# Optimization experiments

Hardware: AMD Instinct MI355X
Metric: run time of the kernel (lower is better)

Reference implementation:

```python
import jax, jax.numpy as jnp
import numpy as np

N_NODES = 50000
N_EDGES = 1600000
D_IN = 64
D_OUT = 64
N_REL = 6


def setup_inputs() -> dict:
    key = jax.random.key(0)
    k = jax.random.split(key, 6)
    x = jax.random.normal(k[0], (N_NODES, D_IN), dtype=jnp.float32)
    edge_index = jax.random.randint(k[1], (2, N_EDGES), 0, N_NODES, dtype=jnp.int32)
    edge_type = jax.random.randint(k[2], (N_EDGES,), 0, N_REL, dtype=jnp.int32)
    # RGCN parameters: per-relation weight, root (self-loop) weight, bias
    W = jax.random.normal(k[3], (N_REL, D_IN, D_OUT), dtype=jnp.float32) / np.float32(np.sqrt(D_IN))
    root = jax.random.normal(k[4], (D_IN, D_OUT), dtype=jnp.float32) / np.float32(np.sqrt(D_IN))
    bias = jnp.zeros((D_OUT,), dtype=jnp.float32)
    return {"x": x, "W": W, "root": root, "bias": bias,
            "edge_index": edge_index, "edge_type": edge_type}


def reference(x, W, root, bias, edge_index, edge_type):
    """RGCNConv forward (PyG semantics, default aggr='mean' per relation):
    out[i] = bias + x[i] @ root + sum_r mean_{j in N_r(i)} (x[j] @ W_r)
    """
    src, dst = edge_index[0], edge_index[1]
    # Transform all node features by all relation weights: [R, N, D_OUT]
    xr = jnp.einsum('nd,rdo->rno', x, W)
    # Per-edge message: relation-specific transformed source feature [E, D_OUT]
    m = xr[edge_type, src]
    # Mean normalization per (dst node, relation): 1 / #relation-r in-edges of dst
    seg = dst.astype(jnp.int32) * N_REL + edge_type.astype(jnp.int32)
    count = jax.ops.segment_sum(jnp.ones((m.shape[0],), x.dtype), seg,
                                num_segments=N_NODES * N_REL)
    norm = jnp.where(count > 0, 1.0 / jnp.maximum(count, 1.0), 0.0)
    m = m * norm[seg][:, None]
    # Scatter-add aggregation over destination nodes
    agg = jax.ops.segment_sum(m, dst, num_segments=N_NODES)
    return agg + x @ root + bias
```

## Files before the change

kernel.cpp:

```cpp
#include <hip/hip_runtime.h>

#define NN 50000
#define NE 1600000
#define D 64
#define NR 6
#define NSEG (NN * NR)
#define SB 512
#define BFRAG_N (4 * 14 * 64 * 8)
#define EPB 6400
#define NBLK1 (NE / EPB)
#define BUKSH 9
#define NBUK ((NSEG + 511) >> 9)
#define NG (NBUK * NBLK1)
#define SNB1 ((NG + SB - 1) / SB)
#define PREPB ((NN * D / 8 + 255) / 256)

typedef __attribute__((ext_vector_type(8))) short short8;
typedef __attribute__((ext_vector_type(4))) float f32x4;

__device__ __forceinline__ unsigned short f2bf(float f) {
    unsigned int u = __float_as_uint(f);
    unsigned int r = (u + 0x7FFF + ((u >> 16) & 1)) >> 16;
    return (unsigned short)r;
}

__global__ __launch_bounds__(256) void prep_hist_k(const float* __restrict__ x,
                                                   const float* __restrict__ W,
                                                   const float* __restrict__ root,
                                                   const int* __restrict__ dsts,
                                                   const int* __restrict__ et,
                                                   int* __restrict__ ghist,
                                                   unsigned short* __restrict__ xh,
                                                   unsigned short* __restrict__ Bfrag) {
    __shared__ int lh[NBUK];
    int tid = threadIdx.x;
    if (blockIdx.x < NBLK1) {
        int blk = blockIdx.x;
        for (int i = tid; i < NBUK; i += 256) lh[i] = 0;
        __syncthreads();
        int base = blk * EPB;
#pragma unroll 5
        for (int i = 0; i < EPB / 256; ++i) {
            int e = base + i * 256 + tid;
            int seg = dsts[e] * NR + et[e];
            atomicAdd(&lh[seg >> BUKSH], 1);
        }
        __syncthreads();
        for (int i = tid; i < NBUK; i += 256) ghist[i * NBLK1 + blk] = lh[i];
    } else {
        int t = (blockIdx.x - NBLK1) * 256 + tid;
        if (t < NN * D / 8) {
            const float4* xp = (const float4*)(x + (size_t)t * 8);
            float4 va = xp[0], vb = xp[1];
            uint4 o;
            o.x = (unsigned int)f2bf(va.x) | ((unsigned int)f2bf(va.y) << 16);
            o.y = (unsigned int)f2bf(va.z) | ((unsigned int)f2bf(va.w) << 16);
            o.z = (unsigned int)f2bf(vb.x) | ((unsigned int)f2bf(vb.y) << 16);
            o.w = (unsigned int)f2bf(vb.z) | ((unsigned int)f2bf(vb.w) << 16);
            *(uint4*)(xh + (size_t)t * 8) = o;
        }
        if (t < BFRAG_N) {
            int j = t & 7;
            int lane = (t >> 3) & 63;
            int rest = t >> 9;
            int ks = rest % 14;
            int nt = rest / 14;
            int k = ks * 32 + ((lane >> 4) * 8) + j;
            int n = nt * 16 + (lane & 15);
            float v = (k < 384) ? W[(size_t)k * 64 + n] : root[(size_t)(k - 384) * 64 + n];
            Bfrag[t] = f2bf(v);
        }
    }
}

__global__ void scanA_k(const int* __restrict__ v, int* __restrict__ incl,
                        int* __restrict__ blocksum, int n) {
    __shared__ int s[SB];
    int t = threadIdx.x, i = blockIdx.x * SB + t;
    s[t] = (i < n) ? v[i] : 0;
    __syncthreads();
    for (int off = 1; off < SB; off <<= 1) {
        int u = (t >= off) ? s[t - off] : 0;
        __syncthreads();
        s[t] += u;
        __syncthreads();
    }
    if (i < n) incl[i] = s[t];
    if (t == SB - 1) blocksum[blockIdx.x] = s[t];
}

__global__ void scanB_k(const int* __restrict__ blocksum, int* __restrict__ blockoff, int nb) {
    __shared__ int s[1024];
    int t = threadIdx.x;
    s[t] = (t < nb) ? blocksum[t] : 0;
    __syncthreads();
    for (int off = 1; off < 1024; off <<= 1) {
        int u = (t >= off) ? s[t - off] : 0;
        __syncthreads();
        s[t] += u;
        __syncthreads();
    }
    if (t < nb) blockoff[t] = s[t];
}

__global__ void scanC2_k(const int* __restrict__ incl, const int* __restrict__ blockoff,
                         const int* __restrict__ v, int* __restrict__ excl, int n) {
    int i = blockIdx.x * blockDim.x + threadIdx.x;
    if (i >= n) return;
    int b = i / SB;
    int Ri = incl[i] + (b > 0 ? blockoff[b - 1] : 0);
    excl[i] = Ri - v[i];
}

__global__ __launch_bounds__(256) void scatter1_k(const int* __restrict__ srcs,
                                                  const int* __restrict__ dsts,
                                                  const int* __restrict__ et,
                                                  const int* __restrict__ goff,
                                                  uint2* __restrict__ kv) {
    __shared__ int cur[NBUK];
    int tid = threadIdx.x, blk = blockIdx.x;
    for (int i = tid; i < NBUK; i += 256) cur[i] = goff[i * NBLK1 + blk];
    __syncthreads();
    int base = blk * EPB;
#pragma unroll 5
    for (int i = 0; i < EPB / 256; ++i) {
        int e = base + i * 256 + tid;
        int seg = dsts[e] * NR + et[e];
        int pos = atomicAdd(&cur[seg >> BUKSH], 1);
        kv[pos] = make_uint2((unsigned int)srcs[e] << 7, (unsigned int)seg);
    }
}

__global__ __launch_bounds__(256) void bucket2_k(const uint2* __restrict__ kv,
                                                 const int* __restrict__ goff,
                                                 int* __restrict__ rowstart,
                                                 int* __restrict__ pay) {
    __shared__ int h[512];
    __shared__ int part[256];
    int tid = threadIdx.x, b = blockIdx.x;
    int base = goff[b * NBLK1];
    int end  = (b + 1 < NBUK) ? goff[(b + 1) * NBLK1] : NE;
    for (int i = tid; i < 512; i += 256) h[i] = 0;
    __syncthreads();
    for (int k = base + tid; k < end; k += 256)
        atomicAdd(&h[kv[k].y & 511], 1);
    __syncthreads();
    int c0 = h[2 * tid], c1 = h[2 * tid + 1];
    part[tid] = c0 + c1;
    __syncthreads();
    for (int off = 1; off < 256; off <<= 1) {
        int u = (tid >= off) ? part[tid - off] : 0;
        __syncthreads();
        part[tid] += u;
        __syncthreads();
    }
    int pbase = (tid > 0) ? part[tid - 1] : 0;
    __syncthreads();
    int e0 = pbase, e1 = pbase + c0;
    h[2 * tid] = e0; h[2 * tid + 1] = e1;
    int segb = b << BUKSH;
    if (segb + 2 * tid     < NSEG) rowstart[segb + 2 * tid]     = base + e0;
    if (segb + 2 * tid + 1 < NSEG) rowstart[segb + 2 * tid + 1] = base + e1;
    if (b == 0 && tid == 0) rowstart[NSEG] = NE;
    __syncthreads();
    for (int k = base + tid; k < end; k += 256) {
        uint2 v = kv[k];
        int pos = base + atomicAdd(&h[v.y & 511], 1);
        pay[pos] = (int)v.x;
    }
}

__global__ __launch_bounds__(256) void agg13_k(const unsigned short* __restrict__ xh,
                                               const int* __restrict__ rowstart,
                                               const int* __restrict__ pay,
                                               unsigned short* __restrict__ Amain) {
    int wv = (blockIdx.x * blockDim.x + threadIdx.x) >> 6;
    int lane = threadIdx.x & 63;
    int g = lane >> 3;
    int q = lane & 7;
    int seg = 8 * wv + g;
    int k0 = rowstart[seg], k1 = rowstart[seg + 1];
    const char* xb = (const char*)xh;
    unsigned int qo = (unsigned int)q << 4;
    float a0 = 0.f, a1 = 0.f, a2 = 0.f, a3 = 0.f;
    float a4 = 0.f, a5 = 0.f, a6 = 0.f, a7 = 0.f;
    int len = k1 - k0;
    int k = k0;
    int k4 = k0 + (len & ~3);
    for (; k < k4; k += 4) {
        unsigned int pv[4];
#pragma unroll
        for (int j = 0; j < 4; ++j) pv[j] = (unsigned int)pay[k + j];
        uint4 uv[4];
#pragma unroll
        for (int j = 0; j < 4; ++j)
            uv[j] = *(const uint4*)(xb + pv[j] + qo);
#pragma unroll
        for (int j = 0; j < 4; ++j) {
            a0 += __uint_as_float(uv[j].x << 16);
            a1 += __uint_as_float(uv[j].x & 0xFFFF0000u);
            a2 += __uint_as_float(uv[j].y << 16);
            a3 += __uint_as_float(uv[j].y & 0xFFFF0000u);
            a4 += __uint_as_float(uv[j].z << 16);
            a5 += __uint_as_float(uv[j].z & 0xFFFF0000u);
            a6 += __uint_as_float(uv[j].w << 16);
            a7 += __uint_as_float(uv[j].w & 0xFFFF0000u);
        }
    }
    if (k < k1) {
        unsigned int pv[3];
        float mv[3];
#pragma unroll
        for (int j = 0; j < 3; ++j) {
            int kk = k + j;
            bool v = kk < k1;
            mv[j] = v ? 1.0f : 0.0f;
            pv[j] = (unsigned int)pay[v ? kk : k];
        }
#pragma unroll
        for (int j = 0; j < 3; ++j) {
            uint4 u = *(const uint4*)(xb + pv[j] + qo);
            a0 += __uint_as_float(u.x << 16) * mv[j];
            a1 += __uint_as_float(u.x & 0xFFFF0000u) * mv[j];
            a2 += __uint_as_float(u.y << 16) * mv[j];
            a3 += __uint_as_float(u.y & 0xFFFF0000u) * mv[j];
            a4 += __uint_as_float(u.z << 16) * mv[j];
            a5 += __uint_as_float(u.z & 0xFFFF0000u) * mv[j];
            a6 += __uint_as_float(u.w << 16) * mv[j];
            a7 += __uint_as_float(u.w & 0xFFFF0000u) * mv[j];
        }
    }
    float nrm = (len > 0) ? 1.0f / (float)len : 0.0f;
    uint4 o;
    o.x = (unsigned int)f2bf(a0 * nrm) | ((unsigned int)f2bf(a1 * nrm) << 16);
    o.y = (unsigned int)f2bf(a2 * nrm) | ((unsigned int)f2bf(a3 * nrm) << 16);
    o.z = (unsigned int)f2bf(a4 * nrm) | ((unsigned int)f2bf(a5 * nrm) << 16);
    o.w = (unsigned int)f2bf(a6 * nrm) | ((unsigned int)f2bf(a7 * nrm) << 16);
    *(uint4*)((char*)Amain + (size_t)seg * 128 + qo) = o;
}

__global__ __launch_bounds__(256) void mix4_k(const unsigned short* __restrict__ Amain,
                                              const unsigned short* __restrict__ xh,
                                              const unsigned short* __restrict__ Bfrag,
                                              const float* __restrict__ bias,
                                              float* __restrict__ out) {
    int t = threadIdx.x;
    int lane = t & 63;
    int w = t >> 6;
    int rowb = blockIdx.x * 64 + w * 16;
    int arow = rowb + (lane & 15);
    if (arow >= NN) arow = NN - 1;
    int ko = (lane >> 4) * 8;
    const unsigned short* ap = Amain + (size_t)arow * 384 + ko;
    const unsigned short* xp = xh + (size_t)arow * 64 + ko;
    const short8* bp = (const short8*)Bfrag + lane;
    f32x4 acc0 = {0.f, 0.f, 0.f, 0.f};
    f32x4 acc1 = acc0, acc2 = acc0, acc3 = acc0;
#pragma unroll
    for (int ks = 0; ks < 14; ++ks) {
        short8 a = (ks < 12) ? *(const short8*)(ap + ks * 32)
                             : *(const short8*)(xp + (ks - 12) * 32);
        short8 b0 = bp[(0 * 14 + ks) * 64];
        short8 b1 = bp[(1 * 14 + ks) * 64];
        short8 b2 = bp[(2 * 14 + ks) * 64];
        short8 b3 = bp[(3 * 14 + ks) * 64];
        acc0 = __builtin_amdgcn_mfma_f32_16x16x32_bf16(a, b0, acc0, 0, 0, 0);
        acc1 = __builtin_amdgcn_mfma_f32_16x16x32_bf16(a, b1, acc1, 0, 0, 0);
        acc2 = __builtin_amdgcn_mfma_f32_16x16x32_bf16(a, b2, acc2, 0, 0, 0);
        acc3 = __builtin_amdgcn_mfma_f32_16x16x32_bf16(a, b3, acc3, 0, 0, 0);
    }
    int col = lane & 15;
    int rout = rowb + (lane >> 4) * 4;
    float bv0 = bias[0 * 16 + col];
    float bv1 = bias[1 * 16 + col];
    float bv2 = bias[2 * 16 + col];
    float bv3 = bias[3 * 16 + col];
#pragma unroll
    for (int j = 0; j < 4; ++j) {
        int rr = rout + j;
        if (rr < NN) {
            float* op = out + (size_t)rr * 64;
            op[0 * 16 + col] = acc0[j] + bv0;
            op[1 * 16 + col] = acc1[j] + bv1;
            op[2 * 16 + col] = acc2[j] + bv2;
            op[3 * 16 + col] = acc3[j] + bv3;
        }
    }
}

__global__ void zero_i32_k(int* __restrict__ p, int n) {
    int i = blockIdx.x * blockDim.x + threadIdx.x;
    if (i < n) p[i] = 0;
}

__global__ void count_edges_k(const int* __restrict__ dst, const int* __restrict__ et,
                              int* __restrict__ cnt) {
    int e = blockIdx.x * blockDim.x + threadIdx.x;
    if (e < NE) atomicAdd(&cnt[dst[e] * NR + et[e]], 1);
}

__global__ void make_norm_k(const int* __restrict__ cnt, float* __restrict__ norm, int n) {
    int i = blockIdx.x * blockDim.x + threadIdx.x;
    if (i < n) {
        int c = cnt[i];
        norm[i] = (c > 0) ? 1.0f / (float)c : 0.0f;
    }
}

__global__ void init_out_k(const float* __restrict__ x, const float* __restrict__ root,
                           const float* __restrict__ bias, float* __restrict__ out) {
    int t = blockIdx.x * blockDim.x + threadIdx.x;
    int n = t >> 6;
    int o = t & 63;
    if (n >= NN) return;
    const float* xrow = x + n * D;
    float acc = bias[o];
#pragma unroll
    for (int d = 0; d < D; ++d) acc = fmaf(xrow[d], root[d * D + o], acc);
    out[t] = acc;
}

__global__ void scatter_mv_k(const int* __restrict__ srcs, const int* __restrict__ dsts,
                             const int* __restrict__ et, const float* __restrict__ x,
                             const float* __restrict__ W, const float* __restrict__ norm,
                             float* __restrict__ out) {
    int t = blockIdx.x * blockDim.x + threadIdx.x;
    int e = t >> 6;
    int o = t & 63;
    if (e >= NE) return;
    int s = srcs[e];
    int d2 = dsts[e];
    int r = et[e];
    float nrm = norm[d2 * NR + r];
    const float* xrow = x + s * D;
    const float* Wr = W + r * D * D + o;
    float acc = 0.0f;
#pragma unroll
    for (int d = 0; d < D; ++d) acc = fmaf(xrow[d], Wr[d * D], acc);
    atomicAdd(&out[d2 * D + o], acc * nrm);
}

extern "C" void kernel_launch(void* const* d_in, const int* in_sizes, int n_in,
                              void* d_out, int out_size, void* d_ws, size_t ws_size,
                              hipStream_t stream) {
    const float* x    = (const float*)d_in[0];
    const float* W    = (const float*)d_in[1];
    const float* root = (const float*)d_in[2];
    const float* bias = (const float*)d_in[3];
    const int*   ei   = (const int*)d_in[4];
    const int*   et   = (const int*)d_in[5];
    float* out = (float*)d_out;
    const int* srcs = ei;
    const int* dsts = ei + NE;

    char* ws = (char*)d_ws;
    size_t off = 0;
    int*   rowstart = (int*)(ws + off); off += (size_t)(NSEG + 1) * 4;
    int*   pay      = (int*)(ws + off); off += (size_t)NE * 4;
    off = (off + 255) & ~(size_t)255;
    uint2* kv       = (uint2*)(ws + off); off += (size_t)NE * 8;
    int*   ghist    = (int*)(ws + off); off += (size_t)NG * 4;
    int*   incl     = (int*)(ws + off); off += (size_t)NG * 4;
    int*   goff     = (int*)(ws + off); off += (size_t)NG * 4;
    int*   blocksum = (int*)(ws + off); off += (size_t)SNB1 * 4;
    int*   blockoff = (int*)(ws + off); off += (size_t)SNB1 * 4;
    off = (off + 255) & ~(size_t)255;
    unsigned short* Bfrag = (unsigned short*)(ws + off); off += (size_t)BFRAG_N * 2;
    off = (off + 255) & ~(size_t)255;
    unsigned short* xh = (unsigned short*)(ws + off); off += (size_t)NN * D * 2;
    off = (off + 255) & ~(size_t)255;
    unsigned short* Amain = (unsigned short*)(ws + off); off += (size_t)NN * 384 * 2;
    bool big = ws_size >= off;

    if (big) {
        prep_hist_k<<<NBLK1 + PREPB, 256, 0, stream>>>(x, W, root, dsts, et, ghist, xh, Bfrag);
        scanA_k<<<SNB1, SB, 0, stream>>>(ghist, incl, blocksum, NG);
        scanB_k<<<1, 1024, 0, stream>>>(blocksum, blockoff, SNB1);
        scanC2_k<<<(NG + 255) / 256, 256, 0, stream>>>(incl, blockoff, ghist, goff, NG);
        scatter1_k<<<NBLK1, 256, 0, stream>>>(srcs, dsts, et, goff, kv);
        bucket2_k<<<NBUK, 256, 0, stream>>>(kv, goff, rowstart, pay);
        int aggwaves = NSEG / 8;
        agg13_k<<<((size_t)aggwaves * 64 + 255) / 256, 256, 0, stream>>>(xh, rowstart, pay, Amain);
        mix4_k<<<(NN + 63) / 64, 256, 0, stream>>>(Amain, xh, Bfrag, bias, out);
    } else {
        int* cnt2  = (int*)(ws);
        float* norm = (float*)(ws + (size_t)NSEG * 4);
        zero_i32_k<<<(NSEG + 255) / 256, 256, 0, stream>>>(cnt2, NSEG);
        count_edges_k<<<(NE + 255) / 256, 256, 0, stream>>>(dsts, et, cnt2);
        make_norm_k<<<(NSEG + 255) / 256, 256, 0, stream>>>(cnt2, norm, NSEG);
        init_out_k<<<((size_t)NN * 64 + 255) / 256, 256, 0, stream>>>(x, root, bias, out);
        scatter_mv_k<<<((size_t)NE * 64 + 255) / 256, 256, 0, stream>>>(srcs, dsts, et, x, W, norm, out);
    }
}
```

Before: 96.75 us.

## Halve bucket width and process 16 segments per wave in aggregation

Bucket size for the two-level counting sort drops from 512 to 256 segments, which doubles the bucket count and makes each bucket2 block use one histogram slot per thread. The aggregation kernel now gives each segment to 4 lanes, each loading two 16-byte chunks, so one wave covers 16 segments instead of 8. This targets divergence from uneven segment lengths and raises memory-level parallelism per lane. In exchange it uses more registers per lane, doubles the number of global histogram groups to scan, and lengthens the scan path.

```diff
diff --git a/kernel.cpp b/kernel.cpp
--- a/kernel.cpp
+++ b/kernel.cpp
@@ -9,11 +9,12 @@
 #define BFRAG_N (4 * 14 * 64 * 8)
 #define EPB 6400
 #define NBLK1 (NE / EPB)
-#define BUKSH 9
-#define NBUK ((NSEG + 511) >> 9)
+#define BUKSH 8
+#define NBUK ((NSEG + 255) >> 8)
 #define NG (NBUK * NBLK1)
 #define SNB1 ((NG + SB - 1) / SB)
 #define PREPB ((NN * D / 8 + 255) / 256)
+#define AGGW (NSEG / 16)
 
 typedef __attribute__((ext_vector_type(8))) short short8;
 typedef __attribute__((ext_vector_type(4))) float f32x4;
@@ -23,6 +24,8 @@
     unsigned int r = (u + 0x7FFF + ((u >> 16) & 1)) >> 16;
     return (unsigned short)r;
 }
+__device__ __forceinline__ float bflo(unsigned int w) { return __uint_as_float(w << 16); }
+__device__ __forceinline__ float bfhi(unsigned int w) { return __uint_as_float(w & 0xFFFF0000u); }
 
 __global__ __launch_bounds__(256) void prep_hist_k(const float* __restrict__ x,
                                                    const float* __restrict__ W,
@@ -135,18 +138,18 @@
                                                  const int* __restrict__ goff,
                                                  int* __restrict__ rowstart,
                                                  int* __restrict__ pay) {
-    __shared__ int h[512];
+    __shared__ int h[256];
     __shared__ int part[256];
     int tid = threadIdx.x, b = blockIdx.x;
     int base = goff[b * NBLK1];
     int end  = (b + 1 < NBUK) ? goff[(b + 1) * NBLK1] : NE;
-    for (int i = tid; i < 512; i += 256) h[i] = 0;
+    h[tid] = 0;
     __syncthreads();
     for (int k = base + tid; k < end; k += 256)
-        atomicAdd(&h[kv[k].y & 511], 1);
-    __syncthreads();
-    int c0 = h[2 * tid], c1 = h[2 * tid + 1];
-    part[tid] = c0 + c1;
+        atomicAdd(&h[kv[k].y & 255], 1);
+    __syncthreads();
+    int c0 = h[tid];
+    part[tid] = c0;
     __syncthreads();
     for (int off = 1; off < 256; off <<= 1) {
         int u = (tid >= off) ? part[tid - off] : 0;
@@ -154,36 +157,36 @@
         part[tid] += u;
         __syncthreads();
     }
-    int pbase = (tid > 0) ? part[tid - 1] : 0;
-    __syncthreads();
-    int e0 = pbase, e1 = pbase + c0;
-    h[2 * tid] = e0; h[2 * tid + 1] = e1;
+    int e0 = part[tid] - c0;
+    __syncthreads();
+    h[tid] = e0;
     int segb = b << BUKSH;
-    if (segb + 2 * tid     < NSEG) rowstart[segb + 2 * tid]     = base + e0;
-    if (segb + 2 * tid + 1 < NSEG) rowstart[segb + 2 * tid + 1] = base + e1;
+    if (segb + tid < NSEG) rowstart[segb + tid] = base + e0;
     if (b == 0 && tid == 0) rowstart[NSEG] = NE;
     __syncthreads();
     for (int k = base + tid; k < end; k += 256) {
         uint2 v = kv[k];
-        int pos = base + atomicAdd(&h[v.y & 511], 1);
+        int pos = base + atomicAdd(&h[v.y & 255], 1);
         pay[pos] = (int)v.x;
     }
 }
 
-__global__ __launch_bounds__(256) void agg13_k(const unsigned short* __restrict__ xh,
+__global__ __launch_bounds__(256) void agg14_k(const unsigned short* __restrict__ xh,
                                                const int* __restrict__ rowstart,
                                                const int* __restrict__ pay,
                                                unsigned short* __restrict__ Amain) {
     int wv = (blockIdx.x * blockDim.x + threadIdx.x) >> 6;
+    if (wv >= AGGW) return;
     int lane = threadIdx.x & 63;
-    int g = lane >> 3;
-    int q = lane & 7;
-    int seg = 8 * wv + g;
+    int g = lane >> 2;
+    int q = lane & 3;
+    int seg = 16 * wv + g;
     int k0 = rowstart[seg], k1 = rowstart[seg + 1];
     const char* xb = (const char*)xh;
-    unsigned int qo = (unsigned int)q << 4;
-    float a0 = 0.f, a1 = 0.f, a2 = 0.f, a3 = 0.f;
-    float a4 = 0.f, a5 = 0.f, a6 = 0.f, a7 = 0.f;
+    unsigned int qo = (unsigned int)q << 5;
+    float acc[16];
+#pragma unroll
+    for (int c = 0; c < 16; ++c) acc[c] = 0.f;
     int len = k1 - k0;
     int k = k0;
     int k4 = k0 + (len & ~3);
@@ -191,20 +194,22 @@
         unsigned int pv[4];
 #pragma unroll
         for (int j = 0; j < 4; ++j) pv[j] = (unsigned int)pay[k + j];
-        uint4 uv[4];
-#pragma unroll
-        for (int j = 0; j < 4; ++j)
+        uint4 uv[4], vv[4];
+#pragma unroll
+        for (int j = 0; j < 4; ++j) {
             uv[j] = *(const uint4*)(xb + pv[j] + qo);
+            vv[j] = *(const uint4*)(xb + pv[j] + qo + 16);
+        }
 #pragma unroll
         for (int j = 0; j < 4; ++j) {
-            a0 += __uint_as_float(uv[j].x << 16);
-            a1 += __uint_as_float(uv[j].x & 0xFFFF0000u);
-            a2 += __uint_as_float(uv[j].y << 16);
-            a3 += __uint_as_float(uv[j].y & 0xFFFF0000u);
-            a4 += __uint_as_float(uv[j].z << 16);
-            a5 += __uint_as_float(uv[j].z & 0xFFFF0000u);
-            a6 += __uint_as_float(uv[j].w << 16);
-            a7 += __uint_as_float(uv[j].w & 0xFFFF0000u);
+            acc[0]  += bflo(uv[j].x); acc[1]  += bfhi(uv[j].x);
+            acc[2]  += bflo(uv[j].y); acc[3]  += bfhi(uv[j].y);
+            acc[4]  += bflo(uv[j].z); acc[5]  += bfhi(uv[j].z);
+            acc[6]  += bflo(uv[j].w); acc[7]  += bfhi(uv[j].w);
+            acc[8]  += bflo(vv[j].x); acc[9]  += bfhi(vv[j].x);
+            acc[10] += bflo(vv[j].y); acc[11] += bfhi(vv[j].y);
+            acc[12] += bflo(vv[j].z); acc[13] += bfhi(vv[j].z);
+            acc[14] += bflo(vv[j].w); acc[15] += bfhi(vv[j].w);
         }
     }
     if (k < k1) {
@@ -220,23 +225,30 @@
 #pragma unroll
         for (int j = 0; j < 3; ++j) {
             uint4 u = *(const uint4*)(xb + pv[j] + qo);
-            a0 += __uint_as_float(u.x << 16) * mv[j];
-            a1 += __uint_as_float(u.x & 0xFFFF0000u) * mv[j];
-            a2 += __uint_as_float(u.y << 16) * mv[j];
-            a3 += __uint_as_float(u.y & 0xFFFF0000u) * mv[j];
-            a4 += __uint_as_float(u.z << 16) * mv[j];
-            a5 += __uint_as_float(u.z & 0xFFFF0000u) * mv[j];
-            a6 += __uint_as_float(u.w << 16) * mv[j];
-            a7 += __uint_as_float(u.w & 0xFFFF0000u) * mv[j];
+            uint4 v2 = *(const uint4*)(xb + pv[j] + qo + 16);
+            acc[0]  += bflo(u.x) * mv[j];  acc[1]  += bfhi(u.x) * mv[j];
+            acc[2]  += bflo(u.y) * mv[j];  acc[3]  += bfhi(u.y) * mv[j];
+            acc[4]  += bflo(u.z) * mv[j];  acc[5]  += bfhi(u.z) * mv[j];
+            acc[6]  += bflo(u.w) * mv[j];  acc[7]  += bfhi(u.w) * mv[j];
+            acc[8]  += bflo(v2.x) * mv[j]; acc[9]  += bfhi(v2.x) * mv[j];
+            acc[10] += bflo(v2.y) * mv[j]; acc[11] += bfhi(v2.y) * mv[j];
+            acc[12] += bflo(v2.z) * mv[j]; acc[13] += bfhi(v2.z) * mv[j];
+            acc[14] += bflo(v2.w) * mv[j]; acc[15] += bfhi(v2.w) * mv[j];
         }
     }
     float nrm = (len > 0) ? 1.0f / (float)len : 0.0f;
-    uint4 o;
-    o.x = (unsigned int)f2bf(a0 * nrm) | ((unsigned int)f2bf(a1 * nrm) << 16);
-    o.y = (unsigned int)f2bf(a2 * nrm) | ((unsigned int)f2bf(a3 * nrm) << 16);
-    o.z = (unsigned int)f2bf(a4 * nrm) | ((unsigned int)f2bf(a5 * nrm) << 16);
-    o.w = (unsigned int)f2bf(a6 * nrm) | ((unsigned int)f2bf(a7 * nrm) << 16);
-    *(uint4*)((char*)Amain + (size_t)seg * 128 + qo) = o;
+    uint4 o, p;
+    o.x = (unsigned int)f2bf(acc[0] * nrm)  | ((unsigned int)f2bf(acc[1] * nrm) << 16);
+    o.y = (unsigned int)f2bf(acc[2] * nrm)  | ((unsigned int)f2bf(acc[3] * nrm) << 16);
+    o.z = (unsigned int)f2bf(acc[4] * nrm)  | ((unsigned int)f2bf(acc[5] * nrm) << 16);
+    o.w = (unsigned int)f2bf(acc[6] * nrm)  | ((unsigned int)f2bf(acc[7] * nrm) << 16);
+    p.x = (unsigned int)f2bf(acc[8] * nrm)  | ((unsigned int)f2bf(acc[9] * nrm) << 16);
+    p.y = (unsigned int)f2bf(acc[10] * nrm) | ((unsigned int)f2bf(acc[11] * nrm) << 16);
+    p.z = (unsigned int)f2bf(acc[12] * nrm) | ((unsigned int)f2bf(acc[13] * nrm) << 16);
+    p.w = (unsigned int)f2bf(acc[14] * nrm) | ((unsigned int)f2bf(acc[15] * nrm) << 16);
+    char* ob = (char*)Amain + (size_t)seg * 128 + qo;
+    *(uint4*)ob = o;
+    *(uint4*)(ob + 16) = p;
 }
 
 __global__ __launch_bounds__(256) void mix4_k(const unsigned short* __restrict__ Amain,
@@ -379,8 +391,7 @@
         scanC2_k<<<(NG + 255) / 256, 256, 0, stream>>>(incl, blockoff, ghist, goff, NG);
         scatter1_k<<<NBLK1, 256, 0, stream>>>(srcs, dsts, et, goff, kv);
         bucket2_k<<<NBUK, 256, 0, stream>>>(kv, goff, rowstart, pay);
-        int aggwaves = NSEG / 8;
-        agg13_k<<<((size_t)aggwaves * 64 + 255) / 256, 256, 0, stream>>>(xh, rowstart, pay, Amain);
+        agg14_k<<<((size_t)AGGW * 64 + 255) / 256, 256, 0, stream>>>(xh, rowstart, pay, Amain);
         mix4_k<<<(NN + 63) / 64, 256, 0, stream>>>(Amain, xh, Bfrag, bias, out);
     } else {
         int* cnt2  = (int*)(ws);
```

New measurement: 100.00 us. 1.03x slower.
